# Kernel optimization log

Hardware: AMD Instinct MI355X
Metric: run time of the kernel (lower is better)

## Reference

```python
import jax, jax.numpy as jnp
import numpy as np

N = 100000
NEG_SLOPE = 0.2
ALPHA = 0.5


def _glorot(key, shape):
    fan_in, fan_out = shape[0], shape[-1]
    lim = jnp.sqrt(6.0 / (fan_in + fan_out))
    return jax.random.uniform(key, shape, jnp.float32, -lim, lim)


def setup_inputs() -> dict:
    key = jax.random.key(0)
    ks = jax.random.split(key, 16)
    x = jax.random.normal(ks[0], (N, 512), jnp.float32)
    spatial_edge_index = jax.random.randint(ks[1], (2, 800000), 0, N, jnp.int64)
    gene_sim_edge_index = jax.random.randint(ks[2], (2, 800000), 0, N, jnp.int64)
    # spatial GAT params (in=512 -> hid=256)
    W_sp = _glorot(ks[3], (512, 256)); a_src_sp = _glorot(ks[4], (256,)); a_dst_sp = _glorot(ks[5], (256,)); b_sp = jnp.zeros((256,), jnp.float32)
    # gene-sim GAT params
    W_gs = _glorot(ks[6], (512, 256)); a_src_gs = _glorot(ks[7], (256,)); a_dst_gs = _glorot(ks[8], (256,)); b_gs = jnp.zeros((256,), jnp.float32)
    # fusion GAT params (hid=256 -> out=64)
    W_fu = _glorot(ks[9], (256, 64)); a_src_fu = _glorot(ks[10], (64,)); a_dst_fu = _glorot(ks[11], (64,)); b_fu = jnp.zeros((64,), jnp.float32)
    return {"x": x, "spatial_edge_index": spatial_edge_index, "gene_sim_edge_index": gene_sim_edge_index,
            "W_sp": W_sp, "a_src_sp": a_src_sp, "a_dst_sp": a_dst_sp, "b_sp": b_sp,
            "W_gs": W_gs, "a_src_gs": a_src_gs, "a_dst_gs": a_dst_gs, "b_gs": b_gs,
            "W_fu": W_fu, "a_src_fu": a_src_fu, "a_dst_fu": a_dst_fu, "b_fu": b_fu}


def gat_conv(x, edge_index, W, a_src, a_dst, bias):
    """PyG GATConv, heads=1, concat=False, add_self_loops=True."""
    n = x.shape[0]
    h = x @ W  # [N, H]
    loops = jnp.arange(n, dtype=edge_index.dtype)
    src = jnp.concatenate([edge_index[0], loops])  # message source j
    dst = jnp.concatenate([edge_index[1], loops])  # aggregation target i
    e = jax.nn.leaky_relu((h @ a_src)[src] + (h @ a_dst)[dst], NEG_SLOPE)  # [E+N]
    # segment softmax over incoming edges of each dst node
    m = jax.ops.segment_max(e, dst, num_segments=n)
    ex = jnp.exp(e - m[dst])
    denom = jax.ops.segment_sum(ex, dst, num_segments=n)
    coef = ex / denom[dst]
    out = jax.ops.segment_sum(coef[:, None] * h[src], dst, num_segments=n)
    return out + bias


def reference(x, spatial_edge_index, gene_sim_edge_index,
              W_sp, a_src_sp, a_dst_sp, b_sp,
              W_gs, a_src_gs, a_dst_gs, b_gs,
              W_fu, a_src_fu, a_dst_fu, b_fu):
    h_spatial = jax.nn.elu(gat_conv(x, spatial_edge_index, W_sp, a_src_sp, a_dst_sp, b_sp))
    h_gene = jax.nn.elu(gat_conv(x, gene_sim_edge_index, W_gs, a_src_gs, a_dst_gs, b_gs))
    h_fused = ALPHA * h_gene + (1.0 - ALPHA) * h_spatial
    return gat_conv(h_fused, spatial_edge_index, W_fu, a_src_fu, a_dst_fu, b_fu)
```

## Files before the change

kernel.cpp:

```cpp
#include <hip/hip_runtime.h>
#include <math.h>


#define NEG_SLOPE 0.2f

typedef __attribute__((ext_vector_type(8))) short bf16x8;
typedef __attribute__((ext_vector_type(4))) float f32x4;

__device__ __forceinline__ unsigned short f2bf(float f) {
  unsigned int u = __float_as_uint(f);
  u = (u + 0x7FFFu + ((u >> 16) & 1u)) >> 16;
  return (unsigned short)u;
}
__device__ __forceinline__ float bf2f(unsigned short u) {
  return __uint_as_float((unsigned int)u << 16);
}
__device__ __forceinline__ int rl_i(int v, int l) {
  return __builtin_amdgcn_readlane(v, l);
}
__device__ __forceinline__ float rl_f(float v, int l) {
  return __uint_as_float(__builtin_amdgcn_readlane(__float_as_uint(v), l));
}

#define GLOAD16(g, l)                                                   \
  __builtin_amdgcn_global_load_lds(                                     \
      (const __attribute__((address_space(1))) void*)(g),               \
      (__attribute__((address_space(3))) void*)(l), 16, 0, 0)

__global__ __launch_bounds__(256) void wt_bf16_all(const float* __restrict__ W_sp,
                                                   const float* __restrict__ W_gs,
                                                   const float* __restrict__ W_fu,
                                                   unsigned short* __restrict__ wt_sp,
                                                   unsigned short* __restrict__ wt_gs,
                                                   unsigned short* __restrict__ wt_fu) {
  const int i = blockIdx.x * 256 + threadIdx.x;
  if (i < 131072) {
    const int k = i >> 8, n = i & 255;
    wt_sp[n * 512 + k] = f2bf(W_sp[i]);
  } else if (i < 262144) {
    const int j = i - 131072;
    const int k = j >> 8, n = j & 255;
    wt_gs[n * 512 + k] = f2bf(W_gs[j]);
  } else if (i < 278528) {
    const int j = i - 262144;
    const int k = j >> 6, n = j & 63;
    wt_fu[n * 256 + k] = f2bf(W_fu[j]);
  }
}

__global__ __launch_bounds__(256) void hist2(const int* __restrict__ dst_sp,
                                             const int* __restrict__ dst_gs,
                                             int* __restrict__ deg_sp,
                                             int* __restrict__ deg_gs, int E) {
  const int m = blockIdx.x * 256 + threadIdx.x;
  if (m < E) {
    atomicAdd(&deg_sp[dst_sp[m]], 1);
    atomicAdd(&deg_gs[dst_gs[m]], 1);
  }
}

__global__ __launch_bounds__(256) void scan1_2(const int* __restrict__ deg_sp,
                                               const int* __restrict__ deg_gs,
                                               int* __restrict__ rs_sp,
                                               int* __restrict__ rs_gs,
                                               int* __restrict__ parts2, int N) {
  __shared__ int sm[256];
  const int* deg = blockIdx.y ? deg_gs : deg_sp;
  int* rs = blockIdx.y ? rs_gs : rs_sp;
  int* parts = parts2 + blockIdx.y * 512;
  const int i = blockIdx.x * 256 + threadIdx.x;
  const int v = (i < N) ? deg[i] : 0;
  sm[threadIdx.x] = v;
  __syncthreads();
  for (int off = 1; off < 256; off <<= 1) {
    const int x = (threadIdx.x >= off) ? sm[threadIdx.x - off] : 0;
    __syncthreads();
    sm[threadIdx.x] += x;
    __syncthreads();
  }
  if (i < N) rs[i] = sm[threadIdx.x] - v;
  if (threadIdx.x == 255) parts[blockIdx.x] = sm[255];
}

__global__ __launch_bounds__(512) void scan2_2(int* __restrict__ parts2, int nb) {
  __shared__ int sm[512];
  int* parts = parts2 + blockIdx.x * 512;
  const int t = threadIdx.x;
  const int v = (t < nb) ? parts[t] : 0;
  sm[t] = v;
  __syncthreads();
  for (int off = 1; off < 512; off <<= 1) {
    const int x = (t >= off) ? sm[t - off] : 0;
    __syncthreads();
    sm[t] += x;
    __syncthreads();
  }
  if (t < nb) parts[t] = sm[t] - v;
}

__global__ __launch_bounds__(256) void scan3_2(int* __restrict__ rs_sp,
                                               int* __restrict__ rs_gs,
                                               const int* __restrict__ parts2,
                                               int N, int E) {
  int* rs = blockIdx.y ? rs_gs : rs_sp;
  const int* parts = parts2 + blockIdx.y * 512;
  const int i = blockIdx.x * 256 + threadIdx.x;
  if (i < N) rs[i] += parts[blockIdx.x];
  if (i == 0) rs[N] = E;
}

__global__ __launch_bounds__(256) void scatter2(const int* __restrict__ ei_sp,
                                                const int* __restrict__ ei_gs,
                                                const int* __restrict__ rs_sp,
                                                const int* __restrict__ rs_gs,
                                                int* __restrict__ cur_sp,
                                                int* __restrict__ cur_gs,
                                                int* __restrict__ csr_sp,
                                                int* __restrict__ csr_gs, int E) {
  const int m = blockIdx.x * 256 + threadIdx.x;
  if (m >= E) return;
  {
    const int s = ei_sp[m], d = ei_sp[E + m];
    csr_sp[rs_sp[d] + atomicAdd(&cur_sp[d], 1)] = s;
  }
  {
    const int s = ei_gs[m], d = ei_gs[E + m];
    csr_gs[rs_gs[d] + atomicAdd(&cur_gs[d], 1)] = s;
  }
}

__global__ __launch_bounds__(512) void gemm2_fused(const float* __restrict__ x,
                                                   const unsigned short* __restrict__ wsp,
                                                   const unsigned short* __restrict__ wgs,
                                                   unsigned short* __restrict__ hb_sp,
                                                   unsigned short* __restrict__ hb_gs,
                                                   int M) {
  __shared__ unsigned short sA[64 * 64];
  __shared__ unsigned short sW[2][256 * 64];
  const int tid = threadIdx.x;
  const int w = tid >> 6, l = tid & 63;
  const int whalf = w >> 2;
  const int wq = w & 3;
  const int bm = blockIdx.x * 64;

  const int arow0 = tid >> 4;
  const int acol4 = (tid & 15) * 4;
  const unsigned short* __restrict__ wtp = whalf ? wgs : wsp;
  const int wrow_in_ch = l >> 3;
  const int wbyte = ((l & 7) * 16) ^ ((wrow_in_ch & 7) << 4);

  f32x4 acc[4][4] = {};
  for (int k0 = 0; k0 < 512; k0 += 64) {
    __syncthreads();
#pragma unroll
    for (int r = 0; r < 2; ++r) {
      const int row = arow0 + r * 32;
      int grow = bm + row;
      grow = grow < M ? grow : M - 1;
      const float4 v = *(const float4*)(x + (size_t)grow * 512 + k0 + acol4);
      ushort4 o;
      o.x = f2bf(v.x); o.y = f2bf(v.y); o.z = f2bf(v.z); o.w = f2bf(v.w);
      const int byte = (row * 128 + acol4 * 2) ^ ((row & 7) << 4);
      *(ushort4*)(((char*)sA) + byte) = o;
    }
#pragma unroll
    for (int c = 0; c < 8; ++c) {
      const int ch = c * 4 + wq;
      const int grow = ch * 8 + wrow_in_ch;
      const char* g = (const char*)wtp + (size_t)grow * 1024 + (size_t)k0 * 2 + wbyte;
      GLOAD16(g, ((char*)sW[whalf]) + ch * 1024);
    }
    __syncthreads();
#pragma unroll
    for (int ks = 0; ks < 2; ++ks) {
      const int cb = ks * 64 + (l >> 4) * 16;
      bf16x8 af[4], bf[4];
#pragma unroll
      for (int m = 0; m < 4; ++m) {
        const int r = m * 16 + (l & 15);
        af[m] = *(const bf16x8*)(((const char*)sA) + r * 128 + (cb ^ ((r & 7) << 4)));
      }
#pragma unroll
      for (int n = 0; n < 4; ++n) {
        const int r = wq * 64 + n * 16 + (l & 15);
        bf[n] = *(const bf16x8*)(((const char*)sW[whalf]) + r * 128 + (cb ^ ((r & 7) << 4)));
      }
#pragma unroll
      for (int m = 0; m < 4; ++m)
#pragma unroll
        for (int n = 0; n < 4; ++n)
          acc[m][n] = __builtin_amdgcn_mfma_f32_16x16x32_bf16(af[m], bf[n], acc[m][n], 0, 0, 0);
    }
  }
  unsigned short* __restrict__ outp = whalf ? hb_gs : hb_sp;
#pragma unroll
  for (int m = 0; m < 4; ++m) {
#pragma unroll
    for (int r = 0; r < 4; ++r) {
      const int row = bm + m * 16 + (l >> 4) * 4 + r;
      if (row < M) {
#pragma unroll
        for (int n = 0; n < 4; ++n)
          outp[(size_t)row * 256 + wq * 64 + n * 16 + (l & 15)] = f2bf(acc[m][n][r]);
      }
    }
  }
}

template <int BN>
__global__ __launch_bounds__(256) void gemm_bf16_nt(const unsigned short* __restrict__ A,
                                                    const unsigned short* __restrict__ Bt,
                                                    unsigned short* __restrict__ C,
                                                    int M, int Nc, int K) {
  constexpr int BM = 128, BK = 64;
  constexpr int NW = BN / 64;
  constexpr int MW = 4 / NW;
  constexpr int MF = (BM / MW) / 16;
  constexpr int NF = 4;
  constexpr int ACW = (BM * BK * 2 / 1024) / 4;
  constexpr int BCW = (BN * BK * 2 / 1024) / 4;
  __shared__ unsigned short sA[BM * BK];
  __shared__ unsigned short sB[BN * BK];
  const int tid = threadIdx.x;
  const int w = tid >> 6, l = tid & 63;
  const int wr = w / NW, wc = w % NW;
  const int bm = blockIdx.x * BM;
  const int bn = blockIdx.y * BN;
  const int crow = l >> 3;
  const int cbyte = (l & 7) * 16;

  f32x4 acc[MF][NF] = {};
  for (int k0 = 0; k0 < K; k0 += BK) {
    __syncthreads();
#pragma unroll
    for (int c = 0; c < ACW; ++c) {
      const int ch = w * ACW + c;
      int row = bm + ch * 8 + crow;
      row = row < M ? row : M - 1;
      const char* g = (const char*)A + (size_t)row * K * 2 + (size_t)k0 * 2 + cbyte;
      GLOAD16(g, ((char*)sA) + ch * 1024);
    }
#pragma unroll
    for (int c = 0; c < BCW; ++c) {
      const int ch = w * BCW + c;
      const int row = bn + ch * 8 + crow;
      const char* g = (const char*)Bt + (size_t)row * K * 2 + (size_t)k0 * 2 + cbyte;
      GLOAD16(g, ((char*)sB) + ch * 1024);
    }
    __syncthreads();
#pragma unroll
    for (int ks = 0; ks < 2; ++ks) {
      bf16x8 af[MF], bfr[NF];
#pragma unroll
      for (int m = 0; m < MF; ++m) {
        const int r = wr * (BM / MW) + m * 16 + (l & 15);
        af[m] = *(const bf16x8*)&sA[r * BK + ks * 32 + (l >> 4) * 8];
      }
#pragma unroll
      for (int n = 0; n < NF; ++n) {
        const int r = wc * 64 + n * 16 + (l & 15);
        bfr[n] = *(const bf16x8*)&sB[r * BK + ks * 32 + (l >> 4) * 8];
      }
#pragma unroll
      for (int m = 0; m < MF; ++m)
#pragma unroll
        for (int n = 0; n < NF; ++n)
          acc[m][n] = __builtin_amdgcn_mfma_f32_16x16x32_bf16(af[m], bfr[n], acc[m][n], 0, 0, 0);
    }
  }
#pragma unroll
  for (int m = 0; m < MF; ++m) {
#pragma unroll
    for (int r = 0; r < 4; ++r) {
      const int row = bm + wr * (BM / MW) + m * 16 + (l >> 4) * 4 + r;
      if (row < M) {
#pragma unroll
        for (int n = 0; n < NF; ++n)
          C[(size_t)row * Nc + bn + wc * 64 + n * 16 + (l & 15)] = f2bf(acc[m][n][r]);
      }
    }
  }
}

__global__ __launch_bounds__(256) void alpha2_256(const ushort4* __restrict__ hsp,
                                                  const ushort4* __restrict__ hgs,
                                                  const float* __restrict__ av_sp_s,
                                                  const float* __restrict__ av_sp_d,
                                                  const float* __restrict__ av_gs_s,
                                                  const float* __restrict__ av_gs_d,
                                                  float* __restrict__ asrc_sp,
                                                  float* __restrict__ adst_sp,
                                                  float* __restrict__ asrc_gs,
                                                  float* __restrict__ adst_gs, int N) {
  const int wave = (int)((blockIdx.x * (size_t)blockDim.x + threadIdx.x) >> 6);
  const int lane = threadIdx.x & 63;
  if (wave >= N) return;
  const ushort4 h1 = hsp[(size_t)wave * 64 + lane];
  const ushort4 h2 = hgs[(size_t)wave * 64 + lane];
  const float4 s1 = ((const float4*)av_sp_s)[lane];
  const float4 d1 = ((const float4*)av_sp_d)[lane];
  const float4 s2 = ((const float4*)av_gs_s)[lane];
  const float4 d2 = ((const float4*)av_gs_d)[lane];
  const float a0 = bf2f(h1.x), a1 = bf2f(h1.y), a2 = bf2f(h1.z), a3 = bf2f(h1.w);
  const float b0 = bf2f(h2.x), b1 = bf2f(h2.y), b2 = bf2f(h2.z), b3 = bf2f(h2.w);
  float p0 = a0 * s1.x + a1 * s1.y + a2 * s1.z + a3 * s1.w;
  float p1 = a0 * d1.x + a1 * d1.y + a2 * d1.z + a3 * d1.w;
  float p2 = b0 * s2.x + b1 * s2.y + b2 * s2.z + b3 * s2.w;
  float p3 = b0 * d2.x + b1 * d2.y + b2 * d2.z + b3 * d2.w;
#pragma unroll
  for (int off = 32; off; off >>= 1) {
    p0 += __shfl_down(p0, off);
    p1 += __shfl_down(p1, off);
    p2 += __shfl_down(p2, off);
    p3 += __shfl_down(p3, off);
  }
  if (lane == 0) {
    asrc_sp[wave] = p0; adst_sp[wave] = p1;
    asrc_gs[wave] = p2; adst_gs[wave] = p3;
  }
}

__global__ __launch_bounds__(256) void alpha64(const unsigned short* __restrict__ h,
                                               const float* __restrict__ a_src,
                                               const float* __restrict__ a_dst,
                                               float* __restrict__ asrc,
                                               float* __restrict__ adst, int N) {
  const int wave = (int)((blockIdx.x * (size_t)blockDim.x + threadIdx.x) >> 6);
  const int lane = threadIdx.x & 63;
  if (wave >= N) return;
  const float hv = bf2f(h[(size_t)wave * 64 + lane]);
  float ps = hv * a_src[lane];
  float pd = hv * a_dst[lane];
#pragma unroll
  for (int off = 32; off; off >>= 1) {
    ps += __shfl_down(ps, off);
    pd += __shfl_down(pd, off);
  }
  if (lane == 0) { asrc[wave] = ps; adst[wave] = pd; }
}

template <int EPI>
__global__ __launch_bounds__(256) void agg_csr256(const int* __restrict__ rs,
                                                  const int* __restrict__ csr,
                                                  const float* __restrict__ asrc,
                                                  const float* __restrict__ adst,
                                                  const ushort4* __restrict__ h4,
                                                  const float* __restrict__ bias,
                                                  const ushort4* __restrict__ other16,
                                                  ushort4* __restrict__ out16, int N) {
  const int d = (int)((blockIdx.x * (size_t)blockDim.x + threadIdx.x) >> 6);
  const int lane = threadIdx.x & 63;
  if (d >= N) return;
  const float ad = adst[d];

  float e = asrc[d] + ad;
  e = e > 0.f ? e : NEG_SLOPE * e;
  const float wself = expf(e);
  float denl = (lane == 0) ? wself : 0.f;
  const ushort4 hv = h4[(size_t)d * 64 + lane];
  float ax = wself * bf2f(hv.x), ay = wself * bf2f(hv.y),
        az = wself * bf2f(hv.z), aw = wself * bf2f(hv.w);

  const int base = rs[d], mend = rs[d + 1];
  for (int c = base; c < mend; c += 64) {
    const int m = c + lane;
    int s = 0;
    float w = 0.f;
    if (m < mend) {
      s = csr[m];
      float e2 = asrc[s] + ad;
      e2 = e2 > 0.f ? e2 : NEG_SLOPE * e2;
      w = expf(e2);
    }
    denl += w;
    const int cnt = min(64, mend - c);
    int j = 0;
    for (; j + 3 < cnt; j += 4) {
      const int s0 = rl_i(s, j), s1 = rl_i(s, j + 1), s2 = rl_i(s, j + 2), s3 = rl_i(s, j + 3);
      const float w0 = rl_f(w, j), w1 = rl_f(w, j + 1), w2 = rl_f(w, j + 2), w3 = rl_f(w, j + 3);
      const ushort4 a0 = h4[(size_t)s0 * 64 + lane];
      const ushort4 a1 = h4[(size_t)s1 * 64 + lane];
      const ushort4 a2 = h4[(size_t)s2 * 64 + lane];
      const ushort4 a3 = h4[(size_t)s3 * 64 + lane];
      ax += w0 * bf2f(a0.x) + w1 * bf2f(a1.x) + w2 * bf2f(a2.x) + w3 * bf2f(a3.x);
      ay += w0 * bf2f(a0.y) + w1 * bf2f(a1.y) + w2 * bf2f(a2.y) + w3 * bf2f(a3.y);
      az += w0 * bf2f(a0.z) + w1 * bf2f(a1.z) + w2 * bf2f(a2.z) + w3 * bf2f(a3.z);
      aw += w0 * bf2f(a0.w) + w1 * bf2f(a1.w) + w2 * bf2f(a2.w) + w3 * bf2f(a3.w);
    }
    for (; j < cnt; ++j) {
      const int sj = rl_i(s, j);
      const float wj = rl_f(w, j);
      const ushort4 aj = h4[(size_t)sj * 64 + lane];
      ax += wj * bf2f(aj.x);
      ay += wj * bf2f(aj.y);
      az += wj * bf2f(aj.z);
      aw += wj * bf2f(aj.w);
    }
  }
#pragma unroll
  for (int off = 32; off; off >>= 1) denl += __shfl_xor(denl, off);
  const float inv = 1.f / denl;

  const float4 b4 = ((const float4*)bias)[lane];
  float v[4] = {ax * inv + b4.x, ay * inv + b4.y, az * inv + b4.z, aw * inv + b4.w};
#pragma unroll
  for (int j = 0; j < 4; ++j) v[j] = v[j] > 0.f ? v[j] : (expf(v[j]) - 1.f);
  ushort4 pk;
  if (EPI == 2) {
    const ushort4 ov = other16[(size_t)d * 64 + lane];
    pk.x = f2bf(0.5f * v[0] + 0.5f * bf2f(ov.x));
    pk.y = f2bf(0.5f * v[1] + 0.5f * bf2f(ov.y));
    pk.z = f2bf(0.5f * v[2] + 0.5f * bf2f(ov.z));
    pk.w = f2bf(0.5f * v[3] + 0.5f * bf2f(ov.w));
  } else {
    pk.x = f2bf(v[0]); pk.y = f2bf(v[1]); pk.z = f2bf(v[2]); pk.w = f2bf(v[3]);
  }
  out16[(size_t)d * 64 + lane] = pk;
}

__global__ __launch_bounds__(256) void agg_csr64(const int* __restrict__ rs,
                                                 const int* __restrict__ csr,
                                                 const float* __restrict__ asrc,
                                                 const float* __restrict__ adst,
                                                 const unsigned short* __restrict__ h,
                                                 const float* __restrict__ bias,
                                                 float* __restrict__ outb, int N) {
  const int d = (int)((blockIdx.x * (size_t)blockDim.x + threadIdx.x) >> 6);
  const int lane = threadIdx.x & 63;
  if (d >= N) return;
  const float ad = adst[d];

  float e = asrc[d] + ad;
  e = e > 0.f ? e : NEG_SLOPE * e;
  const float wself = expf(e);
  float denl = (lane == 0) ? wself : 0.f;
  float acc = wself * bf2f(h[(size_t)d * 64 + lane]);

  const int base = rs[d], mend = rs[d + 1];
  for (int c = base; c < mend; c += 64) {
    const int m = c + lane;
    int s = 0;
    float w = 0.f;
    if (m < mend) {
      s = csr[m];
      float e2 = asrc[s] + ad;
      e2 = e2 > 0.f ? e2 : NEG_SLOPE * e2;
      w = expf(e2);
    }
    denl += w;
    const int cnt = min(64, mend - c);
    int j = 0;
    for (; j + 3 < cnt; j += 4) {
      const int s0 = rl_i(s, j), s1 = rl_i(s, j + 1), s2 = rl_i(s, j + 2), s3 = rl_i(s, j + 3);
      const float w0 = rl_f(w, j), w1 = rl_f(w, j + 1), w2 = rl_f(w, j + 2), w3 = rl_f(w, j + 3);
      const float a0 = bf2f(h[(size_t)s0 * 64 + lane]);
      const float a1 = bf2f(h[(size_t)s1 * 64 + lane]);
      const float a2 = bf2f(h[(size_t)s2 * 64 + lane]);
      const float a3 = bf2f(h[(size_t)s3 * 64 + lane]);
      acc += w0 * a0 + w1 * a1 + w2 * a2 + w3 * a3;
    }
    for (; j < cnt; ++j) {
      const int sj = rl_i(s, j);
      const float wj = rl_f(w, j);
      acc += wj * bf2f(h[(size_t)sj * 64 + lane]);
    }
  }
#pragma unroll
  for (int off = 32; off; off >>= 1) denl += __shfl_xor(denl, off);
  outb[(size_t)d * 64 + lane] = acc / denl + bias[lane];
}

extern "C" void kernel_launch(void* const* d_in, const int* in_sizes, int n_in,
                              void* d_out, int out_size, void* d_ws, size_t ws_size,
                              hipStream_t stream) {
  const float* x        = (const float*)d_in[0];
  const int*   ei_sp    = (const int*)d_in[1];
  const int*   ei_gs    = (const int*)d_in[2];
  const float* W_sp     = (const float*)d_in[3];
  const float* a_src_sp = (const float*)d_in[4];
  const float* a_dst_sp = (const float*)d_in[5];
  const float* b_sp     = (const float*)d_in[6];
  const float* W_gs     = (const float*)d_in[7];
  const float* a_src_gs = (const float*)d_in[8];
  const float* a_dst_gs = (const float*)d_in[9];
  const float* b_gs     = (const float*)d_in[10];
  const float* W_fu     = (const float*)d_in[11];
  const float* a_src_fu = (const float*)d_in[12];
  const float* a_dst_fu = (const float*)d_in[13];
  const float* b_fu     = (const float*)d_in[14];
  float* out = (float*)d_out;

  const int N = in_sizes[0] / 512;
  const int E = in_sizes[1] / 2;
  const int nb = (N + 255) / 256;

  unsigned short* wt_sp = (unsigned short*)d_ws;
  unsigned short* wt_gs = wt_sp + 256 * 512;
  unsigned short* wt_fu = wt_gs + 256 * 512;
  unsigned short* hb_sp = wt_fu + 64 * 256;
  unsigned short* hb_gs = hb_sp + (size_t)N * 256;
  unsigned short* B3    = hb_gs + (size_t)N * 256;
  unsigned short* hfb   = B3 + (size_t)N * 256;
  float* asrc_sp = (float*)(hfb + (size_t)N * 256);
  float* adst_sp = asrc_sp + N;
  float* asrc_gs = adst_sp + N;
  float* adst_gs = asrc_gs + N;
  int* rs_sp  = (int*)(adst_gs + N);
  int* rs_gs  = rs_sp + (N + 1);
  int* csr_sp = rs_gs + (N + 1);
  int* csr_gs = csr_sp + E;
  int* deg_sp = csr_gs + E;
  int* deg_gs = deg_sp + N;
  int* parts2 = deg_gs + N;

  unsigned short* hfu = B3;

  const int BLK = 256;
  const int eGrid = (E + BLK - 1) / BLK;
  const int nodeWaveGrid = (N + 3) / 4;
  const dim3 gFu((N + 127) / 128, 1);

  hipMemsetAsync(deg_sp, 0, (size_t)2 * N * 4, stream);
  hist2<<<eGrid, BLK, 0, stream>>>(ei_sp + E, ei_gs + E, deg_sp, deg_gs, E);
  scan1_2<<<dim3(nb, 2), BLK, 0, stream>>>(deg_sp, deg_gs, rs_sp, rs_gs, parts2, N);
  scan2_2<<<2, 512, 0, stream>>>(parts2, nb);
  scan3_2<<<dim3(nb, 2), BLK, 0, stream>>>(rs_sp, rs_gs, parts2, N, E);
  hipMemsetAsync(deg_sp, 0, (size_t)2 * N * 4, stream);
  scatter2<<<eGrid, BLK, 0, stream>>>(ei_sp, ei_gs, rs_sp, rs_gs, deg_sp, deg_gs,
                                      csr_sp, csr_gs, E);

  wt_bf16_all<<<(278528 + 255) / 256, BLK, 0, stream>>>(W_sp, W_gs, W_fu,
                                                        wt_sp, wt_gs, wt_fu);

  gemm2_fused<<<(N + 63) / 64, 512, 0, stream>>>(x, wt_sp, wt_gs, hb_sp, hb_gs, N);

  alpha2_256<<<nodeWaveGrid, BLK, 0, stream>>>((const ushort4*)hb_sp,
                                               (const ushort4*)hb_gs,
                                               a_src_sp, a_dst_sp, a_src_gs, a_dst_gs,
                                               asrc_sp, adst_sp, asrc_gs, adst_gs, N);

  agg_csr256<1><<<nodeWaveGrid, BLK, 0, stream>>>(rs_sp, csr_sp, asrc_sp, adst_sp,
                                                  (const ushort4*)hb_sp, b_sp,
                                                  nullptr, (ushort4*)B3, N);

  agg_csr256<2><<<nodeWaveGrid, BLK, 0, stream>>>(rs_gs, csr_gs, asrc_gs, adst_gs,
                                                  (const ushort4*)hb_gs, b_gs,
                                                  (const ushort4*)B3, (ushort4*)hfb, N);

  gemm_bf16_nt<64><<<gFu, BLK, 0, stream>>>(hfb, wt_fu, hfu, N, 64, 256);
  alpha64<<<nodeWaveGrid, BLK, 0, stream>>>(hfu, a_src_fu, a_dst_fu,
                                            asrc_sp, adst_sp, N);
  agg_csr64<<<nodeWaveGrid, BLK, 0, stream>>>(rs_sp, csr_sp, asrc_sp, adst_sp,
                                              hfu, b_fu, out, N);
}
```

Baseline: 527.3 us.

## Reuse histogram atomic ordinals for CSR scatter and prefetch GEMM A tiles

The histogram kernel now stores the return value of each degree atomicAdd as the edge's slot within its destination row. The scatter kernel then writes CSR entries without a second round of atomics and without the extra memset. Separately, the fused GEMM register-prefetches the next x tile from global memory while the MFMA work on the current tile runs, which hides the fp32 load latency. The cost is an extra 2*E int buffer in workspace and more register pressure in the GEMM.

```diff
diff --git a/kernel.cpp b/kernel.cpp
--- a/kernel.cpp
+++ b/kernel.cpp
@@ -51,11 +51,13 @@
 __global__ __launch_bounds__(256) void hist2(const int* __restrict__ dst_sp,
                                              const int* __restrict__ dst_gs,
                                              int* __restrict__ deg_sp,
-                                             int* __restrict__ deg_gs, int E) {
+                                             int* __restrict__ deg_gs,
+                                             int* __restrict__ ord_sp,
+                                             int* __restrict__ ord_gs, int E) {
   const int m = blockIdx.x * 256 + threadIdx.x;
   if (m < E) {
-    atomicAdd(&deg_sp[dst_sp[m]], 1);
-    atomicAdd(&deg_gs[dst_gs[m]], 1);
+    ord_sp[m] = atomicAdd(&deg_sp[dst_sp[m]], 1);
+    ord_gs[m] = atomicAdd(&deg_gs[dst_gs[m]], 1);
   }
 }
 
@@ -113,20 +115,14 @@
                                                 const int* __restrict__ ei_gs,
                                                 const int* __restrict__ rs_sp,
                                                 const int* __restrict__ rs_gs,
-                                                int* __restrict__ cur_sp,
-                                                int* __restrict__ cur_gs,
+                                                const int* __restrict__ ord_sp,
+                                                const int* __restrict__ ord_gs,
                                                 int* __restrict__ csr_sp,
                                                 int* __restrict__ csr_gs, int E) {
   const int m = blockIdx.x * 256 + threadIdx.x;
   if (m >= E) return;
-  {
-    const int s = ei_sp[m], d = ei_sp[E + m];
-    csr_sp[rs_sp[d] + atomicAdd(&cur_sp[d], 1)] = s;
-  }
-  {
-    const int s = ei_gs[m], d = ei_gs[E + m];
-    csr_gs[rs_gs[d] + atomicAdd(&cur_gs[d], 1)] = s;
-  }
+  csr_sp[rs_sp[ei_sp[E + m]] + ord_sp[m]] = ei_sp[m];
+  csr_gs[rs_gs[ei_gs[E + m]] + ord_gs[m]] = ei_gs[m];
 }
 
 __global__ __launch_bounds__(512) void gemm2_fused(const float* __restrict__ x,
@@ -145,23 +141,28 @@
 
   const int arow0 = tid >> 4;
   const int acol4 = (tid & 15) * 4;
+  int g0 = bm + arow0;      g0 = g0 < M ? g0 : M - 1;
+  int g1 = bm + arow0 + 32; g1 = g1 < M ? g1 : M - 1;
+  const float* __restrict__ ap0 = x + (size_t)g0 * 512 + acol4;
+  const float* __restrict__ ap1 = x + (size_t)g1 * 512 + acol4;
+  const int abyte0 = (arow0 * 128 + acol4 * 2) ^ ((arow0 & 7) << 4);
+  const int abyte1 = ((arow0 + 32) * 128 + acol4 * 2) ^ (((arow0 + 32) & 7) << 4);
+
   const unsigned short* __restrict__ wtp = whalf ? wgs : wsp;
   const int wrow_in_ch = l >> 3;
   const int wbyte = ((l & 7) * 16) ^ ((wrow_in_ch & 7) << 4);
 
   f32x4 acc[4][4] = {};
+  float4 xr0 = *(const float4*)ap0;
+  float4 xr1 = *(const float4*)ap1;
   for (int k0 = 0; k0 < 512; k0 += 64) {
-    __syncthreads();
-#pragma unroll
-    for (int r = 0; r < 2; ++r) {
-      const int row = arow0 + r * 32;
-      int grow = bm + row;
-      grow = grow < M ? grow : M - 1;
-      const float4 v = *(const float4*)(x + (size_t)grow * 512 + k0 + acol4);
-      ushort4 o;
-      o.x = f2bf(v.x); o.y = f2bf(v.y); o.z = f2bf(v.z); o.w = f2bf(v.w);
-      const int byte = (row * 128 + acol4 * 2) ^ ((row & 7) << 4);
-      *(ushort4*)(((char*)sA) + byte) = o;
+    __builtin_amdgcn_s_barrier();
+    {
+      ushort4 o0, o1;
+      o0.x = f2bf(xr0.x); o0.y = f2bf(xr0.y); o0.z = f2bf(xr0.z); o0.w = f2bf(xr0.w);
+      o1.x = f2bf(xr1.x); o1.y = f2bf(xr1.y); o1.z = f2bf(xr1.z); o1.w = f2bf(xr1.w);
+      *(ushort4*)(((char*)sA) + abyte0) = o0;
+      *(ushort4*)(((char*)sA) + abyte1) = o1;
     }
 #pragma unroll
     for (int c = 0; c < 8; ++c) {
@@ -171,6 +172,11 @@
       GLOAD16(g, ((char*)sW[whalf]) + ch * 1024);
     }
     __syncthreads();
+    if (k0 < 448) {
+      xr0 = *(const float4*)(ap0 + k0 + 64);
+      xr1 = *(const float4*)(ap1 + k0 + 64);
+    }
+    asm volatile("" ::: "memory");
 #pragma unroll
     for (int ks = 0; ks < 2; ++ks) {
       const int cb = ks * 64 + (l >> 4) * 16;
@@ -512,6 +518,8 @@
   int* deg_sp = csr_gs + E;
   int* deg_gs = deg_sp + N;
   int* parts2 = deg_gs + N;
+  int* ord_sp = parts2 + 1024;
+  int* ord_gs = ord_sp + E;
 
   unsigned short* hfu = B3;
 
@@ -521,12 +529,12 @@
   const dim3 gFu((N + 127) / 128, 1);
 
   hipMemsetAsync(deg_sp, 0, (size_t)2 * N * 4, stream);
-  hist2<<<eGrid, BLK, 0, stream>>>(ei_sp + E, ei_gs + E, deg_sp, deg_gs, E);
+  hist2<<<eGrid, BLK, 0, stream>>>(ei_sp + E, ei_gs + E, deg_sp, deg_gs,
+                                   ord_sp, ord_gs, E);
   scan1_2<<<dim3(nb, 2), BLK, 0, stream>>>(deg_sp, deg_gs, rs_sp, rs_gs, parts2, N);
   scan2_2<<<2, 512, 0, stream>>>(parts2, nb);
   scan3_2<<<dim3(nb, 2), BLK, 0, stream>>>(rs_sp, rs_gs, parts2, N, E);
-  hipMemsetAsync(deg_sp, 0, (size_t)2 * N * 4, stream);
-  scatter2<<<eGrid, BLK, 0, stream>>>(ei_sp, ei_gs, rs_sp, rs_gs, deg_sp, deg_gs,
+  scatter2<<<eGrid, BLK, 0, stream>>>(ei_sp, ei_gs, rs_sp, rs_gs, ord_sp, ord_gs,
                                       csr_sp, csr_gs, E);
 
   wt_bf16_all<<<(278528 + 255) / 256, BLK, 0, stream>>>(W_sp, W_gs, W_fu,
```

After: 507.5 us. 3.8% less time.

## Fuse attention logit dot products into GEMM epilogues and reuse histogram slots for CSR

Applied to the files above, without the earlier changes.

Computes the per-node source/destination attention scores directly from the MFMA accumulators in both GEMM epilogues, eliminating the separate alpha kernels that reread the hidden features. The degree histogram now records each edge's atomic slot, so the scatter pass skips the second memset and atomic round. This costs extra shuffles and shared-memory reductions in the GEMMs and a workspace array of size 2E. The scores are now computed from fp32 accumulators rather than bf16-rounded features.

```diff
diff --git a/kernel.cpp b/kernel.cpp
--- a/kernel.cpp
+++ b/kernel.cpp
@@ -51,11 +51,13 @@
 __global__ __launch_bounds__(256) void hist2(const int* __restrict__ dst_sp,
                                              const int* __restrict__ dst_gs,
                                              int* __restrict__ deg_sp,
-                                             int* __restrict__ deg_gs, int E) {
+                                             int* __restrict__ deg_gs,
+                                             int* __restrict__ ord_sp,
+                                             int* __restrict__ ord_gs, int E) {
   const int m = blockIdx.x * 256 + threadIdx.x;
   if (m < E) {
-    atomicAdd(&deg_sp[dst_sp[m]], 1);
-    atomicAdd(&deg_gs[dst_gs[m]], 1);
+    ord_sp[m] = atomicAdd(&deg_sp[dst_sp[m]], 1);
+    ord_gs[m] = atomicAdd(&deg_gs[dst_gs[m]], 1);
   }
 }
 
@@ -113,27 +115,29 @@
                                                 const int* __restrict__ ei_gs,
                                                 const int* __restrict__ rs_sp,
                                                 const int* __restrict__ rs_gs,
-                                                int* __restrict__ cur_sp,
-                                                int* __restrict__ cur_gs,
+                                                const int* __restrict__ ord_sp,
+                                                const int* __restrict__ ord_gs,
                                                 int* __restrict__ csr_sp,
                                                 int* __restrict__ csr_gs, int E) {
   const int m = blockIdx.x * 256 + threadIdx.x;
   if (m >= E) return;
-  {
-    const int s = ei_sp[m], d = ei_sp[E + m];
-    csr_sp[rs_sp[d] + atomicAdd(&cur_sp[d], 1)] = s;
-  }
-  {
-    const int s = ei_gs[m], d = ei_gs[E + m];
-    csr_gs[rs_gs[d] + atomicAdd(&cur_gs[d], 1)] = s;
-  }
+  csr_sp[rs_sp[ei_sp[E + m]] + ord_sp[m]] = ei_sp[m];
+  csr_gs[rs_gs[ei_gs[E + m]] + ord_gs[m]] = ei_gs[m];
 }
 
 __global__ __launch_bounds__(512) void gemm2_fused(const float* __restrict__ x,
                                                    const unsigned short* __restrict__ wsp,
                                                    const unsigned short* __restrict__ wgs,
+                                                   const float* __restrict__ avs_sp,
+                                                   const float* __restrict__ avd_sp,
+                                                   const float* __restrict__ avs_gs,
+                                                   const float* __restrict__ avd_gs,
                                                    unsigned short* __restrict__ hb_sp,
                                                    unsigned short* __restrict__ hb_gs,
+                                                   float* __restrict__ asrc_sp,
+                                                   float* __restrict__ adst_sp,
+                                                   float* __restrict__ asrc_gs,
+                                                   float* __restrict__ adst_gs,
                                                    int M) {
   __shared__ unsigned short sA[64 * 64];
   __shared__ unsigned short sW[2][256 * 64];
@@ -205,138 +209,140 @@
       }
     }
   }
-}
-
-template <int BN>
-__global__ __launch_bounds__(256) void gemm_bf16_nt(const unsigned short* __restrict__ A,
-                                                    const unsigned short* __restrict__ Bt,
-                                                    unsigned short* __restrict__ C,
-                                                    int M, int Nc, int K) {
-  constexpr int BM = 128, BK = 64;
-  constexpr int NW = BN / 64;
-  constexpr int MW = 4 / NW;
-  constexpr int MF = (BM / MW) / 16;
-  constexpr int NF = 4;
-  constexpr int ACW = (BM * BK * 2 / 1024) / 4;
-  constexpr int BCW = (BN * BK * 2 / 1024) / 4;
-  __shared__ unsigned short sA[BM * BK];
-  __shared__ unsigned short sB[BN * BK];
+  const float* __restrict__ avs = whalf ? avs_gs : avs_sp;
+  const float* __restrict__ avd = whalf ? avd_gs : avd_sp;
+  float as_v[4], ad_v[4];
+#pragma unroll
+  for (int n = 0; n < 4; ++n) {
+    as_v[n] = avs[wq * 64 + n * 16 + (l & 15)];
+    ad_v[n] = avd[wq * 64 + n * 16 + (l & 15)];
+  }
+  __syncthreads();
+  float* __restrict__ red = (float*)sA;
+#pragma unroll
+  for (int m = 0; m < 4; ++m) {
+#pragma unroll
+    for (int r = 0; r < 4; ++r) {
+      float ps = acc[m][0][r] * as_v[0] + acc[m][1][r] * as_v[1] +
+                 acc[m][2][r] * as_v[2] + acc[m][3][r] * as_v[3];
+      float pd = acc[m][0][r] * ad_v[0] + acc[m][1][r] * ad_v[1] +
+                 acc[m][2][r] * ad_v[2] + acc[m][3][r] * ad_v[3];
+#pragma unroll
+      for (int off = 1; off < 16; off <<= 1) {
+        ps += __shfl_xor(ps, off);
+        pd += __shfl_xor(pd, off);
+      }
+      if ((l & 15) == 0) {
+        const int row = m * 16 + (l >> 4) * 4 + r;
+        red[(((whalf * 4 + wq) * 64) + row) * 2 + 0] = ps;
+        red[(((whalf * 4 + wq) * 64) + row) * 2 + 1] = pd;
+      }
+    }
+  }
+  __syncthreads();
+  if (tid < 128) {
+    const int half = tid >> 6, row = tid & 63;
+    float s = 0.f, d = 0.f;
+#pragma unroll
+    for (int q = 0; q < 4; ++q) {
+      s += red[(((half * 4 + q) * 64) + row) * 2 + 0];
+      d += red[(((half * 4 + q) * 64) + row) * 2 + 1];
+    }
+    const int grow = bm + row;
+    if (grow < M) {
+      if (half == 0) { asrc_sp[grow] = s; adst_sp[grow] = d; }
+      else           { asrc_gs[grow] = s; adst_gs[grow] = d; }
+    }
+  }
+}
+
+__global__ __launch_bounds__(256) void gemm_fu_alpha(const unsigned short* __restrict__ A,
+                                                     const unsigned short* __restrict__ Bt,
+                                                     const float* __restrict__ avs,
+                                                     const float* __restrict__ avd,
+                                                     unsigned short* __restrict__ C,
+                                                     float* __restrict__ asrc,
+                                                     float* __restrict__ adst,
+                                                     int M) {
+  constexpr int K = 256, Nc = 64;
+  __shared__ unsigned short sA[128 * 64];
+  __shared__ unsigned short sB[64 * 64];
   const int tid = threadIdx.x;
   const int w = tid >> 6, l = tid & 63;
-  const int wr = w / NW, wc = w % NW;
-  const int bm = blockIdx.x * BM;
-  const int bn = blockIdx.y * BN;
+  const int bm = blockIdx.x * 128;
   const int crow = l >> 3;
   const int cbyte = (l & 7) * 16;
 
-  f32x4 acc[MF][NF] = {};
-  for (int k0 = 0; k0 < K; k0 += BK) {
-    __syncthreads();
-#pragma unroll
-    for (int c = 0; c < ACW; ++c) {
-      const int ch = w * ACW + c;
+  f32x4 acc[2][4] = {};
+  for (int k0 = 0; k0 < K; k0 += 64) {
+    __syncthreads();
+#pragma unroll
+    for (int c = 0; c < 4; ++c) {
+      const int ch = w * 4 + c;
       int row = bm + ch * 8 + crow;
       row = row < M ? row : M - 1;
       const char* g = (const char*)A + (size_t)row * K * 2 + (size_t)k0 * 2 + cbyte;
       GLOAD16(g, ((char*)sA) + ch * 1024);
     }
 #pragma unroll
-    for (int c = 0; c < BCW; ++c) {
-      const int ch = w * BCW + c;
-      const int row = bn + ch * 8 + crow;
+    for (int c = 0; c < 2; ++c) {
+      const int ch = w * 2 + c;
+      const int row = ch * 8 + crow;
       const char* g = (const char*)Bt + (size_t)row * K * 2 + (size_t)k0 * 2 + cbyte;
       GLOAD16(g, ((char*)sB) + ch * 1024);
     }
     __syncthreads();
 #pragma unroll
     for (int ks = 0; ks < 2; ++ks) {
-      bf16x8 af[MF], bfr[NF];
-#pragma unroll
-      for (int m = 0; m < MF; ++m) {
-        const int r = wr * (BM / MW) + m * 16 + (l & 15);
-        af[m] = *(const bf16x8*)&sA[r * BK + ks * 32 + (l >> 4) * 8];
-      }
-#pragma unroll
-      for (int n = 0; n < NF; ++n) {
-        const int r = wc * 64 + n * 16 + (l & 15);
-        bfr[n] = *(const bf16x8*)&sB[r * BK + ks * 32 + (l >> 4) * 8];
-      }
-#pragma unroll
-      for (int m = 0; m < MF; ++m)
-#pragma unroll
-        for (int n = 0; n < NF; ++n)
+      bf16x8 af[2], bfr[4];
+#pragma unroll
+      for (int m = 0; m < 2; ++m) {
+        const int r = w * 32 + m * 16 + (l & 15);
+        af[m] = *(const bf16x8*)&sA[r * 64 + ks * 32 + (l >> 4) * 8];
+      }
+#pragma unroll
+      for (int n = 0; n < 4; ++n) {
+        const int r = n * 16 + (l & 15);
+        bfr[n] = *(const bf16x8*)&sB[r * 64 + ks * 32 + (l >> 4) * 8];
+      }
+#pragma unroll
+      for (int m = 0; m < 2; ++m)
+#pragma unroll
+        for (int n = 0; n < 4; ++n)
           acc[m][n] = __builtin_amdgcn_mfma_f32_16x16x32_bf16(af[m], bfr[n], acc[m][n], 0, 0, 0);
     }
   }
-#pragma unroll
-  for (int m = 0; m < MF; ++m) {
+  float as_v[4], ad_v[4];
+#pragma unroll
+  for (int n = 0; n < 4; ++n) {
+    as_v[n] = avs[n * 16 + (l & 15)];
+    ad_v[n] = avd[n * 16 + (l & 15)];
+  }
+#pragma unroll
+  for (int m = 0; m < 2; ++m) {
 #pragma unroll
     for (int r = 0; r < 4; ++r) {
-      const int row = bm + wr * (BM / MW) + m * 16 + (l >> 4) * 4 + r;
+      const int row = bm + w * 32 + m * 16 + (l >> 4) * 4 + r;
       if (row < M) {
 #pragma unroll
-        for (int n = 0; n < NF; ++n)
-          C[(size_t)row * Nc + bn + wc * 64 + n * 16 + (l & 15)] = f2bf(acc[m][n][r]);
-      }
-    }
-  }
-}
-
-__global__ __launch_bounds__(256) void alpha2_256(const ushort4* __restrict__ hsp,
-                                                  const ushort4* __restrict__ hgs,
-                                                  const float* __restrict__ av_sp_s,
-                                                  const float* __restrict__ av_sp_d,
-                                                  const float* __restrict__ av_gs_s,
-                                                  const float* __restrict__ av_gs_d,
-                                                  float* __restrict__ asrc_sp,
-                                                  float* __restrict__ adst_sp,
-                                                  float* __restrict__ asrc_gs,
-                                                  float* __restrict__ adst_gs, int N) {
-  const int wave = (int)((blockIdx.x * (size_t)blockDim.x + threadIdx.x) >> 6);
-  const int lane = threadIdx.x & 63;
-  if (wave >= N) return;
-  const ushort4 h1 = hsp[(size_t)wave * 64 + lane];
-  const ushort4 h2 = hgs[(size_t)wave * 64 + lane];
-  const float4 s1 = ((const float4*)av_sp_s)[lane];
-  const float4 d1 = ((const float4*)av_sp_d)[lane];
-  const float4 s2 = ((const float4*)av_gs_s)[lane];
-  const float4 d2 = ((const float4*)av_gs_d)[lane];
-  const float a0 = bf2f(h1.x), a1 = bf2f(h1.y), a2 = bf2f(h1.z), a3 = bf2f(h1.w);
-  const float b0 = bf2f(h2.x), b1 = bf2f(h2.y), b2 = bf2f(h2.z), b3 = bf2f(h2.w);
-  float p0 = a0 * s1.x + a1 * s1.y + a2 * s1.z + a3 * s1.w;
-  float p1 = a0 * d1.x + a1 * d1.y + a2 * d1.z + a3 * d1.w;
-  float p2 = b0 * s2.x + b1 * s2.y + b2 * s2.z + b3 * s2.w;
-  float p3 = b0 * d2.x + b1 * d2.y + b2 * d2.z + b3 * d2.w;
-#pragma unroll
-  for (int off = 32; off; off >>= 1) {
-    p0 += __shfl_down(p0, off);
-    p1 += __shfl_down(p1, off);
-    p2 += __shfl_down(p2, off);
-    p3 += __shfl_down(p3, off);
-  }
-  if (lane == 0) {
-    asrc_sp[wave] = p0; adst_sp[wave] = p1;
-    asrc_gs[wave] = p2; adst_gs[wave] = p3;
-  }
-}
-
-__global__ __launch_bounds__(256) void alpha64(const unsigned short* __restrict__ h,
-                                               const float* __restrict__ a_src,
-                                               const float* __restrict__ a_dst,
-                                               float* __restrict__ asrc,
-                                               float* __restrict__ adst, int N) {
-  const int wave = (int)((blockIdx.x * (size_t)blockDim.x + threadIdx.x) >> 6);
-  const int lane = threadIdx.x & 63;
-  if (wave >= N) return;
-  const float hv = bf2f(h[(size_t)wave * 64 + lane]);
-  float ps = hv * a_src[lane];
-  float pd = hv * a_dst[lane];
-#pragma unroll
-  for (int off = 32; off; off >>= 1) {
-    ps += __shfl_down(ps, off);
-    pd += __shfl_down(pd, off);
-  }
-  if (lane == 0) { asrc[wave] = ps; adst[wave] = pd; }
+        for (int n = 0; n < 4; ++n)
+          C[(size_t)row * Nc + n * 16 + (l & 15)] = f2bf(acc[m][n][r]);
+      }
+      float ps = acc[m][0][r] * as_v[0] + acc[m][1][r] * as_v[1] +
+                 acc[m][2][r] * as_v[2] + acc[m][3][r] * as_v[3];
+      float pd = acc[m][0][r] * ad_v[0] + acc[m][1][r] * ad_v[1] +
+                 acc[m][2][r] * ad_v[2] + acc[m][3][r] * ad_v[3];
+#pragma unroll
+      for (int off = 1; off < 16; off <<= 1) {
+        ps += __shfl_xor(ps, off);
+        pd += __shfl_xor(pd, off);
+      }
+      if ((l & 15) == 0 && row < M) {
+        asrc[row] = ps;
+        adst[row] = pd;
+      }
+    }
+  }
 }
 
 template <int EPI>
@@ -404,7 +410,7 @@
   const float4 b4 = ((const float4*)bias)[lane];
   float v[4] = {ax * inv + b4.x, ay * inv + b4.y, az * inv + b4.z, aw * inv + b4.w};
 #pragma unroll
-  for (int j = 0; j < 4; ++j) v[j] = v[j] > 0.f ? v[j] : (expf(v[j]) - 1.f);
+  for (int j2 = 0; j2 < 4; ++j2) v[j2] = v[j2] > 0.f ? v[j2] : (expf(v[j2]) - 1.f);
   ushort4 pk;
   if (EPI == 2) {
     const ushort4 ov = other16[(size_t)d * 64 + lane];
@@ -512,32 +518,31 @@
   int* deg_sp = csr_gs + E;
   int* deg_gs = deg_sp + N;
   int* parts2 = deg_gs + N;
+  int* ord_sp = parts2 + 1024;
+  int* ord_gs = ord_sp + E;
 
   unsigned short* hfu = B3;
 
   const int BLK = 256;
   const int eGrid = (E + BLK - 1) / BLK;
   const int nodeWaveGrid = (N + 3) / 4;
-  const dim3 gFu((N + 127) / 128, 1);
 
   hipMemsetAsync(deg_sp, 0, (size_t)2 * N * 4, stream);
-  hist2<<<eGrid, BLK, 0, stream>>>(ei_sp + E, ei_gs + E, deg_sp, deg_gs, E);
+  hist2<<<eGrid, BLK, 0, stream>>>(ei_sp + E, ei_gs + E, deg_sp, deg_gs,
+                                   ord_sp, ord_gs, E);
   scan1_2<<<dim3(nb, 2), BLK, 0, stream>>>(deg_sp, deg_gs, rs_sp, rs_gs, parts2, N);
   scan2_2<<<2, 512, 0, stream>>>(parts2, nb);
   scan3_2<<<dim3(nb, 2), BLK, 0, stream>>>(rs_sp, rs_gs, parts2, N, E);
-  hipMemsetAsync(deg_sp, 0, (size_t)2 * N * 4, stream);
-  scatter2<<<eGrid, BLK, 0, stream>>>(ei_sp, ei_gs, rs_sp, rs_gs, deg_sp, deg_gs,
+  scatter2<<<eGrid, BLK, 0, stream>>>(ei_sp, ei_gs, rs_sp, rs_gs, ord_sp, ord_gs,
                                       csr_sp, csr_gs, E);
 
   wt_bf16_all<<<(278528 + 255) / 256, BLK, 0, stream>>>(W_sp, W_gs, W_fu,
                                                         wt_sp, wt_gs, wt_fu);
 
-  gemm2_fused<<<(N + 63) / 64, 512, 0, stream>>>(x, wt_sp, wt_gs, hb_sp, hb_gs, N);
-
-  alpha2_256<<<nodeWaveGrid, BLK, 0, stream>>>((const ushort4*)hb_sp,
-                                               (const ushort4*)hb_gs,
-                                               a_src_sp, a_dst_sp, a_src_gs, a_dst_gs,
-                                               asrc_sp, adst_sp, asrc_gs, adst_gs, N);
+  gemm2_fused<<<(N + 63) / 64, 512, 0, stream>>>(x, wt_sp, wt_gs,
+                                                 a_src_sp, a_dst_sp, a_src_gs, a_dst_gs,
+                                                 hb_sp, hb_gs,
+                                                 asrc_sp, adst_sp, asrc_gs, adst_gs, N);
 
   agg_csr256<1><<<nodeWaveGrid, BLK, 0, stream>>>(rs_sp, csr_sp, asrc_sp, adst_sp,
                                                   (const ushort4*)hb_sp, b_sp,
@@ -547,9 +552,8 @@
                                                   (const ushort4*)hb_gs, b_gs,
                                                   (const ushort4*)B3, (ushort4*)hfb, N);
 
-  gemm_bf16_nt<64><<<gFu, BLK, 0, stream>>>(hfb, wt_fu, hfu, N, 64, 256);
-  alpha64<<<nodeWaveGrid, BLK, 0, stream>>>(hfu, a_src_fu, a_dst_fu,
-                                            asrc_sp, adst_sp, N);
+  gemm_fu_alpha<<<(N + 127) / 128, BLK, 0, stream>>>(hfb, wt_fu, a_src_fu, a_dst_fu,
+                                                     hfu, asrc_sp, adst_sp, N);
   agg_csr64<<<nodeWaveGrid, BLK, 0, stream>>>(rs_sp, csr_sp, asrc_sp, adst_sp,
                                               hfu, b_fu, out, N);
 }
```

Result: faster. 504.7 us (-4.3%).
